# Optimization experiments

Measured on AMD Instinct MI355X. Metric: run time of the kernel, lower is better.

## Reference

```python
import jax, jax.numpy as jnp
import numpy as np

PAD = 1
THRESH = 10.0


def setup_inputs() -> dict:
    key = jax.random.key(0)
    k1, k2, k3 = jax.random.split(key, 3)
    x = jax.random.normal(k1, (8, 16, 62, 62), dtype=jnp.float32)
    W = jax.random.normal(k2, (32, 16, 3, 3), dtype=jnp.float32)
    b = jax.random.normal(k3, (32,), dtype=jnp.float32)
    return {"x": x, "W": W, "b": b}


def reference(x, W, b):
    # ZeroPad2d(padding) on all four sides
    x = jnp.pad(x, ((0, 0), (0, 0), (PAD, PAD), (PAD, PAD)))
    T, C, xr, xc = x.shape
    O, _, wr, wc = W.shape
    L = xr * xc

    # get_xfft_thresh: 1D FFT over flattened HxW, zero coeffs with |Re| < thresh
    xf = jnp.fft.fft(x.reshape(T, C, L))                      # (T,C,L) complex
    xf = jnp.where(jnp.abs(xf.real) < THRESH, jnp.zeros_like(xf), xf)

    # get_Wfft: zero-pad kernel to (xr,xc) bottom/right, flatten, reverse along
    # length (flipud(flip([0,1])) nets to a flip of the last axis only), then FFT
    Wp = jnp.pad(W, ((0, 0), (0, 0), (0, xr - wr), (0, xc - wc))).reshape(O, C, L)
    Wf = jnp.fft.fft(Wp[:, :, ::-1])                          # (O,C,L) complex

    # fftConv1D, batched over (image, out_channel):
    y = jnp.fft.ifft(xf[:, None, :, :] * Wf[None, :, :, :]).real  # (T,O,C,L)
    # torch.roll(y, 1) with no dims rolls the FLATTENED (C*L) tensor by 1
    y = jnp.roll(y.reshape(T, O, C * L), 1, axis=-1).reshape(T, O, C, xr, xc)
    y = y.sum(axis=2)                                         # sum over in-channels
    ans_r, ans_c = xr - wr + 1, xc - wc + 1
    y = y[:, :, :ans_r, :ans_c]
    return y + b[None, :, None, None]
```

## Files before the change

### kernel.cpp

```cpp
#include <hip/hip_runtime.h>
#include <math.h>

#define TWO_PI 6.28318530717958647692f
#define NT     512
#define RPW    8
#define PITCH  65
#define THRESH 10.0f
#define C64    0.995184726672196886f
#define S64    0.098017140329560602f
#define C4096  0.999998823451701879f
#define S4096  0.001533980186284766f

typedef float v2f __attribute__((ext_vector_type(2)));

__device__ __forceinline__ int brev6(int x) {
    return (int)(__brev((unsigned)x) >> 26);
}

__device__ __forceinline__ v2f cmul_add(v2f a, v2f b, v2f acc) {
    acc += (v2f){a.x, a.x} * b;
    acc += (v2f){a.y, a.y} * (v2f){-b.y, b.x};
    return acc;
}

template<int R>
__device__ __forceinline__ void fft64_dif(float (&re)[R], float (&im)[R],
                                          int lane, float sign) {
    #pragma unroll
    for (int h = 32; h >= 1; h >>= 1) {
        int j = lane & (h - 1);
        float ang = sign * (TWO_PI / 64.0f) * (float)(j * (32 / h));
        float wr, wi;
        __sincosf(ang, &wi, &wr);
        bool upper = (lane & h) != 0;
        float cwr = upper ? wr : 1.0f;
        float cwi = upper ? wi : 0.0f;
        float sgn = upper ? -1.0f : 1.0f;
        #pragma unroll
        for (int m = 0; m < R; ++m) {
            float orr = __shfl_xor(re[m], h, 64);
            float oii = __shfl_xor(im[m], h, 64);
            float ar = fmaf(sgn, re[m], orr);
            float ai = fmaf(sgn, im[m], oii);
            re[m] = ar * cwr - ai * cwi;
            im[m] = ar * cwi + ai * cwr;
        }
    }
}

template<int R>
__device__ __forceinline__ void fft64_dit(float (&re)[R], float (&im)[R],
                                          int lane, float sign) {
    #pragma unroll
    for (int h = 1; h <= 32; h <<= 1) {
        int j = lane & (h - 1);
        float ang = sign * (TWO_PI / 64.0f) * (float)(j * (32 / h));
        float wr, wi;
        __sincosf(ang, &wi, &wr);
        bool upper = (lane & h) != 0;
        float cwr = upper ? wr : 1.0f;
        float cwi = upper ? wi : 0.0f;
        float sgn = upper ? -1.0f : 1.0f;
        #pragma unroll
        for (int m = 0; m < R; ++m) {
            float tr = re[m] * cwr - im[m] * cwi;
            float ti = re[m] * cwi + im[m] * cwr;
            float orr = __shfl_xor(tr, h, 64);
            float oii = __shfl_xor(ti, h, 64);
            re[m] = fmaf(sgn, tr, orr);
            im[m] = fmaf(sgn, ti, oii);
        }
    }
}

__global__ __launch_bounds__(NT) void fwdA_kernel(const float* __restrict__ x,
                                                  float2* __restrict__ Xa) {
    __shared__ float sre[64 * 33];
    __shared__ float sim[64 * 33];
    const int task = blockIdx.x >> 1;
    const int h    = blockIdx.x & 1;
    const int tid  = threadIdx.x;
    const int lane = tid & 63;
    const int w    = tid >> 6;
    const float* xr = x + (size_t)task * 62 * 62;
    for (int idx = tid; idx < 64 * 32; idx += NT) {
        int r = idx >> 5, j = idx & 31;
        int n2 = 32 * h + j;
        float v = 0.0f;
        if (r >= 1 && r <= 62 && n2 >= 1 && n2 <= 62)
            v = xr[(r - 1) * 62 + (n2 - 1)];
        sre[r * 33 + j] = v;
    }
    __syncthreads();
    float re[4], im[4];
    #pragma unroll
    for (int m = 0; m < 4; ++m) {
        re[m] = sre[lane * 33 + (w * 4 + m)];
        im[m] = 0.0f;
    }
    fft64_dif<4>(re, im, lane, -1.0f);
    __syncthreads();
    const int k1 = brev6(lane);
    #pragma unroll
    for (int m = 0; m < 4; ++m) {
        int j  = w * 4 + m;
        int n2 = 32 * h + j;
        float cr, ci;
        __sincosf(-(TWO_PI / 4096.0f) * (float)(k1 * n2), &ci, &cr);
        sre[k1 * 33 + j] = re[m] * cr - im[m] * ci;
        sim[k1 * 33 + j] = re[m] * ci + im[m] * cr;
    }
    __syncthreads();
    float2* Arow = Xa + (size_t)task * 4096;
    for (int idx = tid; idx < 64 * 32; idx += NT) {
        int k = idx >> 5, j = idx & 31;
        Arow[k * 64 + 32 * h + j] = make_float2(sre[k * 33 + j], sim[k * 33 + j]);
    }
}

__global__ __launch_bounds__(NT) void fwdB_kernel(const float2* __restrict__ Xa,
                                                  float2* __restrict__ X) {
    const int task = blockIdx.x >> 1;
    const int h    = blockIdx.x & 1;
    const int tid  = threadIdx.x;
    const int lane = tid & 63;
    const int w    = tid >> 6;
    const float2* Arow = Xa + (size_t)task * 4096;
    float re[4], im[4];
    #pragma unroll
    for (int m = 0; m < 4; ++m) {
        float2 xv = Arow[(32 * h + w * 4 + m) * 64 + lane];
        re[m] = xv.x; im[m] = xv.y;
    }
    fft64_dif<4>(re, im, lane, -1.0f);
    float2* Xrow = X + (size_t)task * 4096;
    #pragma unroll
    for (int m = 0; m < 4; ++m) {
        float rr = re[m], ii = im[m];
        if (fabsf(rr) < THRESH) { rr = 0.0f; ii = 0.0f; }
        Xrow[(32 * h + w * 4 + m) * 64 + lane] = make_float2(rr, ii);
    }
}

__global__ __launch_bounds__(NT, 2) void conv_kernel(const float2* __restrict__ X,
                                                     const float* __restrict__ W,
                                                     const float* __restrict__ b,
                                                     float* __restrict__ out) {
    __shared__ float sre[64 * PITCH];
    __shared__ float sim[64 * PITCH];
    const int t    = blockIdx.x >> 5;
    const int o    = blockIdx.x & 31;
    const int tid  = threadIdx.x;
    const int lane = tid & 63;
    const int w    = tid >> 6;

    const int k2 = brev6(lane);
    float elr, eli;
    __sincosf((TWO_PI / 64.0f) * (float)k2, &eli, &elr);

    v2f uv[RPW], vv[RPW], v2v[RPW];
    {
        float cur, cui, cvr, cvi;
        __sincosf((TWO_PI / 8.0f) * (float)w, &cui, &cur);
        __sincosf((TWO_PI / 512.0f) * (float)w, &cvi, &cvr);
        #pragma unroll
        for (int m = 0; m < RPW; ++m) {
            uv[m] = (v2f){cur, cui};
            float vvr = cvr * elr - cvi * eli;
            float vvi = cvr * eli + cvi * elr;
            vv[m]  = (v2f){vvr, vvi};
            v2v[m] = (v2f){vvr * vvr - vvi * vvi, 2.0f * vvr * vvi};
            float nur = cur * C64 - cui * S64;
            cui = cur * S64 + cui * C64; cur = nur;
            float nvr = cvr * C4096 - cvi * S4096;
            cvi = cvr * S4096 + cvi * C4096; cvr = nvr;
        }
    }

    v2f S[RPW];
    #pragma unroll
    for (int m = 0; m < RPW; ++m) S[m] = (v2f){0.0f, 0.0f};

    const float2* Xt = X + (size_t)t * 16 * 4096 + (w * (RPW * 64) + lane);
    const float*  wo = W + o * 144;

    v2f xb[RPW];
    #pragma unroll
    for (int m = 0; m < RPW; ++m) {
        float2 q = Xt[m * 64];
        xb[m] = (v2f){q.x, q.y};
    }
    #pragma unroll 1
    for (int c = 0; c < 16; ++c) {
        v2f xn[RPW];
        if (c < 15) {
            const float2* xp = Xt + (c + 1) * 4096;
            #pragma unroll
            for (int m = 0; m < RPW; ++m) {
                float2 q = xp[m * 64];
                xn[m] = (v2f){q.x, q.y};
            }
        }
        const float wa0 = wo[c*9+0], wa1 = wo[c*9+1], wa2 = wo[c*9+2];
        const float wa3 = wo[c*9+3], wa4 = wo[c*9+4], wa5 = wo[c*9+5];
        const float wa6 = wo[c*9+6], wa7 = wo[c*9+7], wa8 = wo[c*9+8];
        #pragma unroll
        for (int m = 0; m < RPW; ++m) {
            v2f v = vv[m], v2 = v2v[m], u = uv[m];
            v2f h0 = (v2f){wa0, 0.0f}; h0 += v * wa1; h0 += v2 * wa2;
            v2f h1 = (v2f){wa3, 0.0f}; h1 += v * wa4; h1 += v2 * wa5;
            v2f h2 = (v2f){wa6, 0.0f}; h2 += v * wa7; h2 += v2 * wa8;
            v2f in = cmul_add(u, h2, h1);
            v2f P  = cmul_add(u, in, h0);
            S[m]   = cmul_add(xb[m], P, S[m]);
        }
        #pragma unroll
        for (int m = 0; m < RPW; ++m) xb[m] = xn[m];
    }

    float re[RPW], im[RPW];
    #pragma unroll
    for (int m = 0; m < RPW; ++m) { re[m] = S[m].x; im[m] = S[m].y; }
    fft64_dit<RPW>(re, im, lane, +1.0f);
    {
        float cr, ci, sr, si;
        __sincosf((TWO_PI / 512.0f) * (float)(lane * w), &ci, &cr);
        __sincosf((TWO_PI / 4096.0f) * (float)lane, &si, &sr);
        #pragma unroll
        for (int m = 0; m < RPW; ++m) {
            float rr = re[m] * cr - im[m] * ci;
            im[m]    = re[m] * ci + im[m] * cr;
            re[m]    = rr;
            float nr = cr * sr - ci * si;
            ci = cr * si + ci * sr; cr = nr;
        }
    }
    #pragma unroll
    for (int m = 0; m < RPW; ++m) {
        int k1 = w * RPW + m;
        sre[k1 * PITCH + lane] = re[m];
        sim[k1 * PITCH + lane] = im[m];
    }
    __syncthreads();
    #pragma unroll
    for (int m = 0; m < RPW; ++m) {
        int n2 = w * RPW + m;
        re[m] = sre[lane * PITCH + n2];
        im[m] = sim[lane * PITCH + n2];
    }
    fft64_dif<RPW>(re, im, lane, +1.0f);
    __syncthreads();
    const int n1 = brev6(lane);
    #pragma unroll
    for (int m = 0; m < RPW; ++m) {
        int n2 = w * RPW + m;
        sre[n1 * PITCH + n2] = re[m];
    }
    __syncthreads();
    const float bias = b[o];
    float* orow = out + (size_t)blockIdx.x * 62 * 62;
    for (int idx = tid; idx < 62 * 62; idx += NT) {
        int r = idx / 62, s = idx - r * 62;
        orow[idx] = sre[r * PITCH + s] * (1.0f / 4096.0f) + bias;
    }
}

extern "C" void kernel_launch(void* const* d_in, const int* in_sizes, int n_in,
                              void* d_out, int out_size, void* d_ws, size_t ws_size,
                              hipStream_t stream) {
    const float* x = (const float*)d_in[0];
    const float* W = (const float*)d_in[1];
    const float* b = (const float*)d_in[2];
    float* out = (float*)d_out;
    float2* Xa = (float2*)d_ws;
    float2* X  = Xa + 128 * 4096;

    fwdA_kernel<<<dim3(256), dim3(NT), 0, stream>>>(x, Xa);
    fwdB_kernel<<<dim3(256), dim3(NT), 0, stream>>>(Xa, X);
    conv_kernel<<<dim3(256), dim3(NT), 0, stream>>>(X, W, b, out);
}
```

Before: 87.84 us.

## Fuse three FFT-conv stages into one cooperative kernel with grid syncs

Merges the two forward-FFT passes and the convolution/inverse-FFT pass into a single cooperative kernel launched with hipLaunchCooperativeKernel, separated by grid.sync() barriers. This removes two kernel launches and the gaps between them. In exchange it adds the cost of grid-wide barriers, and the shared memory is sized for the largest stage, which could limit occupancy. Correctness relies on all 256 blocks being co-resident.

```diff
diff --git a/kernel.cpp b/kernel.cpp
--- a/kernel.cpp
+++ b/kernel.cpp
@@ -1,5 +1,8 @@
 #include <hip/hip_runtime.h>
+#include <hip/hip_cooperative_groups.h>
 #include <math.h>
+
+namespace cg = cooperative_groups;
 
 #define TWO_PI 6.28318530717958647692f
 #define NT     512
@@ -73,195 +76,194 @@
     }
 }
 
-__global__ __launch_bounds__(NT) void fwdA_kernel(const float* __restrict__ x,
-                                                  float2* __restrict__ Xa) {
-    __shared__ float sre[64 * 33];
-    __shared__ float sim[64 * 33];
-    const int task = blockIdx.x >> 1;
-    const int h    = blockIdx.x & 1;
+__global__ __launch_bounds__(NT, 2) void fused_kernel(const float* __restrict__ x,
+                                                      const float* __restrict__ W,
+                                                      const float* __restrict__ b,
+                                                      float* __restrict__ out,
+                                                      float2* __restrict__ Xa,
+                                                      float2* __restrict__ X) {
+    cg::grid_group grid = cg::this_grid();
+    __shared__ float sre[64 * PITCH];
+    __shared__ float sim[64 * PITCH];
     const int tid  = threadIdx.x;
     const int lane = tid & 63;
     const int w    = tid >> 6;
-    const float* xr = x + (size_t)task * 62 * 62;
-    for (int idx = tid; idx < 64 * 32; idx += NT) {
-        int r = idx >> 5, j = idx & 31;
-        int n2 = 32 * h + j;
-        float v = 0.0f;
-        if (r >= 1 && r <= 62 && n2 >= 1 && n2 <= 62)
-            v = xr[(r - 1) * 62 + (n2 - 1)];
-        sre[r * 33 + j] = v;
-    }
-    __syncthreads();
-    float re[4], im[4];
-    #pragma unroll
-    for (int m = 0; m < 4; ++m) {
-        re[m] = sre[lane * 33 + (w * 4 + m)];
-        im[m] = 0.0f;
-    }
-    fft64_dif<4>(re, im, lane, -1.0f);
-    __syncthreads();
-    const int k1 = brev6(lane);
-    #pragma unroll
-    for (int m = 0; m < 4; ++m) {
-        int j  = w * 4 + m;
-        int n2 = 32 * h + j;
-        float cr, ci;
-        __sincosf(-(TWO_PI / 4096.0f) * (float)(k1 * n2), &ci, &cr);
-        sre[k1 * 33 + j] = re[m] * cr - im[m] * ci;
-        sim[k1 * 33 + j] = re[m] * ci + im[m] * cr;
-    }
-    __syncthreads();
-    float2* Arow = Xa + (size_t)task * 4096;
-    for (int idx = tid; idx < 64 * 32; idx += NT) {
-        int k = idx >> 5, j = idx & 31;
-        Arow[k * 64 + 32 * h + j] = make_float2(sre[k * 33 + j], sim[k * 33 + j]);
-    }
-}
-
-__global__ __launch_bounds__(NT) void fwdB_kernel(const float2* __restrict__ Xa,
-                                                  float2* __restrict__ X) {
-    const int task = blockIdx.x >> 1;
-    const int h    = blockIdx.x & 1;
-    const int tid  = threadIdx.x;
-    const int lane = tid & 63;
-    const int w    = tid >> 6;
-    const float2* Arow = Xa + (size_t)task * 4096;
-    float re[4], im[4];
-    #pragma unroll
-    for (int m = 0; m < 4; ++m) {
-        float2 xv = Arow[(32 * h + w * 4 + m) * 64 + lane];
-        re[m] = xv.x; im[m] = xv.y;
-    }
-    fft64_dif<4>(re, im, lane, -1.0f);
-    float2* Xrow = X + (size_t)task * 4096;
-    #pragma unroll
-    for (int m = 0; m < 4; ++m) {
-        float rr = re[m], ii = im[m];
-        if (fabsf(rr) < THRESH) { rr = 0.0f; ii = 0.0f; }
-        Xrow[(32 * h + w * 4 + m) * 64 + lane] = make_float2(rr, ii);
-    }
-}
-
-__global__ __launch_bounds__(NT, 2) void conv_kernel(const float2* __restrict__ X,
-                                                     const float* __restrict__ W,
-                                                     const float* __restrict__ b,
-                                                     float* __restrict__ out) {
-    __shared__ float sre[64 * PITCH];
-    __shared__ float sim[64 * PITCH];
-    const int t    = blockIdx.x >> 5;
-    const int o    = blockIdx.x & 31;
-    const int tid  = threadIdx.x;
-    const int lane = tid & 63;
-    const int w    = tid >> 6;
-
-    const int k2 = brev6(lane);
-    float elr, eli;
-    __sincosf((TWO_PI / 64.0f) * (float)k2, &eli, &elr);
-
-    v2f uv[RPW], vv[RPW], v2v[RPW];
+
     {
-        float cur, cui, cvr, cvi;
-        __sincosf((TWO_PI / 8.0f) * (float)w, &cui, &cur);
-        __sincosf((TWO_PI / 512.0f) * (float)w, &cvi, &cvr);
-        #pragma unroll
-        for (int m = 0; m < RPW; ++m) {
-            uv[m] = (v2f){cur, cui};
-            float vvr = cvr * elr - cvi * eli;
-            float vvi = cvr * eli + cvi * elr;
-            vv[m]  = (v2f){vvr, vvi};
-            v2v[m] = (v2f){vvr * vvr - vvi * vvi, 2.0f * vvr * vvi};
-            float nur = cur * C64 - cui * S64;
-            cui = cur * S64 + cui * C64; cur = nur;
-            float nvr = cvr * C4096 - cvi * S4096;
-            cvi = cvr * S4096 + cvi * C4096; cvr = nvr;
-        }
-    }
-
-    v2f S[RPW];
-    #pragma unroll
-    for (int m = 0; m < RPW; ++m) S[m] = (v2f){0.0f, 0.0f};
-
-    const float2* Xt = X + (size_t)t * 16 * 4096 + (w * (RPW * 64) + lane);
-    const float*  wo = W + o * 144;
-
-    v2f xb[RPW];
-    #pragma unroll
-    for (int m = 0; m < RPW; ++m) {
-        float2 q = Xt[m * 64];
-        xb[m] = (v2f){q.x, q.y};
-    }
-    #pragma unroll 1
-    for (int c = 0; c < 16; ++c) {
-        v2f xn[RPW];
-        if (c < 15) {
-            const float2* xp = Xt + (c + 1) * 4096;
+        const int task = blockIdx.x >> 1;
+        const int h    = blockIdx.x & 1;
+        const float* xr = x + (size_t)task * 62 * 62;
+        for (int idx = tid; idx < 64 * 32; idx += NT) {
+            int r = idx >> 5, j = idx & 31;
+            int n2 = 32 * h + j;
+            float v = 0.0f;
+            if (r >= 1 && r <= 62 && n2 >= 1 && n2 <= 62)
+                v = xr[(r - 1) * 62 + (n2 - 1)];
+            sre[r * 33 + j] = v;
+        }
+        __syncthreads();
+        float re[4], im[4];
+        #pragma unroll
+        for (int m = 0; m < 4; ++m) {
+            re[m] = sre[lane * 33 + (w * 4 + m)];
+            im[m] = 0.0f;
+        }
+        fft64_dif<4>(re, im, lane, -1.0f);
+        __syncthreads();
+        const int k1 = brev6(lane);
+        #pragma unroll
+        for (int m = 0; m < 4; ++m) {
+            int j  = w * 4 + m;
+            int n2 = 32 * h + j;
+            float cr, ci;
+            __sincosf(-(TWO_PI / 4096.0f) * (float)(k1 * n2), &ci, &cr);
+            sre[k1 * 33 + j] = re[m] * cr - im[m] * ci;
+            sim[k1 * 33 + j] = re[m] * ci + im[m] * cr;
+        }
+        __syncthreads();
+        float2* Arow = Xa + (size_t)task * 4096;
+        for (int idx = tid; idx < 64 * 32; idx += NT) {
+            int k = idx >> 5, j = idx & 31;
+            Arow[k * 64 + 32 * h + j] =
+                make_float2(sre[k * 33 + j], sim[k * 33 + j]);
+        }
+    }
+    grid.sync();
+
+    {
+        const int task = blockIdx.x >> 1;
+        const int h    = blockIdx.x & 1;
+        const float2* Arow = Xa + (size_t)task * 4096;
+        float re[4], im[4];
+        #pragma unroll
+        for (int m = 0; m < 4; ++m) {
+            float2 xv = Arow[(32 * h + w * 4 + m) * 64 + lane];
+            re[m] = xv.x; im[m] = xv.y;
+        }
+        fft64_dif<4>(re, im, lane, -1.0f);
+        float2* Xrow = X + (size_t)task * 4096;
+        #pragma unroll
+        for (int m = 0; m < 4; ++m) {
+            float rr = re[m], ii = im[m];
+            if (fabsf(rr) < THRESH) { rr = 0.0f; ii = 0.0f; }
+            Xrow[(32 * h + w * 4 + m) * 64 + lane] = make_float2(rr, ii);
+        }
+    }
+    grid.sync();
+
+    {
+        const int t    = blockIdx.x >> 5;
+        const int o    = blockIdx.x & 31;
+
+        const int k2 = brev6(lane);
+        float elr, eli;
+        __sincosf((TWO_PI / 64.0f) * (float)k2, &eli, &elr);
+
+        v2f uv[RPW], vv[RPW], v2v[RPW];
+        {
+            float cur, cui, cvr, cvi;
+            __sincosf((TWO_PI / 8.0f) * (float)w, &cui, &cur);
+            __sincosf((TWO_PI / 512.0f) * (float)w, &cvi, &cvr);
             #pragma unroll
             for (int m = 0; m < RPW; ++m) {
-                float2 q = xp[m * 64];
-                xn[m] = (v2f){q.x, q.y};
-            }
-        }
-        const float wa0 = wo[c*9+0], wa1 = wo[c*9+1], wa2 = wo[c*9+2];
-        const float wa3 = wo[c*9+3], wa4 = wo[c*9+4], wa5 = wo[c*9+5];
-        const float wa6 = wo[c*9+6], wa7 = wo[c*9+7], wa8 = wo[c*9+8];
-        #pragma unroll
-        for (int m = 0; m < RPW; ++m) {
-            v2f v = vv[m], v2 = v2v[m], u = uv[m];
-            v2f h0 = (v2f){wa0, 0.0f}; h0 += v * wa1; h0 += v2 * wa2;
-            v2f h1 = (v2f){wa3, 0.0f}; h1 += v * wa4; h1 += v2 * wa5;
-            v2f h2 = (v2f){wa6, 0.0f}; h2 += v * wa7; h2 += v2 * wa8;
-            v2f in = cmul_add(u, h2, h1);
-            v2f P  = cmul_add(u, in, h0);
-            S[m]   = cmul_add(xb[m], P, S[m]);
-        }
-        #pragma unroll
-        for (int m = 0; m < RPW; ++m) xb[m] = xn[m];
-    }
-
-    float re[RPW], im[RPW];
-    #pragma unroll
-    for (int m = 0; m < RPW; ++m) { re[m] = S[m].x; im[m] = S[m].y; }
-    fft64_dit<RPW>(re, im, lane, +1.0f);
-    {
-        float cr, ci, sr, si;
-        __sincosf((TWO_PI / 512.0f) * (float)(lane * w), &ci, &cr);
-        __sincosf((TWO_PI / 4096.0f) * (float)lane, &si, &sr);
-        #pragma unroll
-        for (int m = 0; m < RPW; ++m) {
-            float rr = re[m] * cr - im[m] * ci;
-            im[m]    = re[m] * ci + im[m] * cr;
-            re[m]    = rr;
-            float nr = cr * sr - ci * si;
-            ci = cr * si + ci * sr; cr = nr;
-        }
-    }
-    #pragma unroll
-    for (int m = 0; m < RPW; ++m) {
-        int k1 = w * RPW + m;
-        sre[k1 * PITCH + lane] = re[m];
-        sim[k1 * PITCH + lane] = im[m];
-    }
-    __syncthreads();
-    #pragma unroll
-    for (int m = 0; m < RPW; ++m) {
-        int n2 = w * RPW + m;
-        re[m] = sre[lane * PITCH + n2];
-        im[m] = sim[lane * PITCH + n2];
-    }
-    fft64_dif<RPW>(re, im, lane, +1.0f);
-    __syncthreads();
-    const int n1 = brev6(lane);
-    #pragma unroll
-    for (int m = 0; m < RPW; ++m) {
-        int n2 = w * RPW + m;
-        sre[n1 * PITCH + n2] = re[m];
-    }
-    __syncthreads();
-    const float bias = b[o];
-    float* orow = out + (size_t)blockIdx.x * 62 * 62;
-    for (int idx = tid; idx < 62 * 62; idx += NT) {
-        int r = idx / 62, s = idx - r * 62;
-        orow[idx] = sre[r * PITCH + s] * (1.0f / 4096.0f) + bias;
+                uv[m] = (v2f){cur, cui};
+                float vvr = cvr * elr - cvi * eli;
+                float vvi = cvr * eli + cvi * elr;
+                vv[m]  = (v2f){vvr, vvi};
+                v2v[m] = (v2f){vvr * vvr - vvi * vvi, 2.0f * vvr * vvi};
+                float nur = cur * C64 - cui * S64;
+                cui = cur * S64 + cui * C64; cur = nur;
+                float nvr = cvr * C4096 - cvi * S4096;
+                cvi = cvr * S4096 + cvi * C4096; cvr = nvr;
+            }
+        }
+
+        v2f S[RPW];
+        #pragma unroll
+        for (int m = 0; m < RPW; ++m) S[m] = (v2f){0.0f, 0.0f};
+
+        const float2* Xt = X + (size_t)t * 16 * 4096 + (w * (RPW * 64) + lane);
+        const float*  wo = W + o * 144;
+
+        v2f xb[RPW];
+        #pragma unroll
+        for (int m = 0; m < RPW; ++m) {
+            float2 q = Xt[m * 64];
+            xb[m] = (v2f){q.x, q.y};
+        }
+        #pragma unroll 1
+        for (int c = 0; c < 16; ++c) {
+            v2f xn[RPW];
+            if (c < 15) {
+                const float2* xp = Xt + (c + 1) * 4096;
+                #pragma unroll
+                for (int m = 0; m < RPW; ++m) {
+                    float2 q = xp[m * 64];
+                    xn[m] = (v2f){q.x, q.y};
+                }
+            }
+            const float wa0 = wo[c*9+0], wa1 = wo[c*9+1], wa2 = wo[c*9+2];
+            const float wa3 = wo[c*9+3], wa4 = wo[c*9+4], wa5 = wo[c*9+5];
+            const float wa6 = wo[c*9+6], wa7 = wo[c*9+7], wa8 = wo[c*9+8];
+            #pragma unroll
+            for (int m = 0; m < RPW; ++m) {
+                v2f v = vv[m], v2 = v2v[m], u = uv[m];
+                v2f h0 = (v2f){wa0, 0.0f}; h0 += v * wa1; h0 += v2 * wa2;
+                v2f h1 = (v2f){wa3, 0.0f}; h1 += v * wa4; h1 += v2 * wa5;
+                v2f h2 = (v2f){wa6, 0.0f}; h2 += v * wa7; h2 += v2 * wa8;
+                v2f in = cmul_add(u, h2, h1);
+                v2f P  = cmul_add(u, in, h0);
+                S[m]   = cmul_add(xb[m], P, S[m]);
+            }
+            #pragma unroll
+            for (int m = 0; m < RPW; ++m) xb[m] = xn[m];
+        }
+
+        float re[RPW], im[RPW];
+        #pragma unroll
+        for (int m = 0; m < RPW; ++m) { re[m] = S[m].x; im[m] = S[m].y; }
+        fft64_dit<RPW>(re, im, lane, +1.0f);
+        {
+            float cr, ci, sr, si;
+            __sincosf((TWO_PI / 512.0f) * (float)(lane * w), &ci, &cr);
+            __sincosf((TWO_PI / 4096.0f) * (float)lane, &si, &sr);
+            #pragma unroll
+            for (int m = 0; m < RPW; ++m) {
+                float rr = re[m] * cr - im[m] * ci;
+                im[m]    = re[m] * ci + im[m] * cr;
+                re[m]    = rr;
+                float nr = cr * sr - ci * si;
+                ci = cr * si + ci * sr; cr = nr;
+            }
+        }
+        #pragma unroll
+        for (int m = 0; m < RPW; ++m) {
+            int k1 = w * RPW + m;
+            sre[k1 * PITCH + lane] = re[m];
+            sim[k1 * PITCH + lane] = im[m];
+        }
+        __syncthreads();
+        #pragma unroll
+        for (int m = 0; m < RPW; ++m) {
+            int n2 = w * RPW + m;
+            re[m] = sre[lane * PITCH + n2];
+            im[m] = sim[lane * PITCH + n2];
+        }
+        fft64_dif<RPW>(re, im, lane, +1.0f);
+        __syncthreads();
+        const int n1 = brev6(lane);
+        #pragma unroll
+        for (int m = 0; m < RPW; ++m) {
+            int n2 = w * RPW + m;
+            sre[n1 * PITCH + n2] = re[m];
+        }
+        __syncthreads();
+        const float bias = b[o];
+        float* orow = out + (size_t)blockIdx.x * 62 * 62;
+        for (int idx = tid; idx < 62 * 62; idx += NT) {
+            int r = idx / 62, s = idx - r * 62;
+            orow[idx] = sre[r * PITCH + s] * (1.0f / 4096.0f) + bias;
+        }
     }
 }
 
@@ -275,7 +277,8 @@
     float2* Xa = (float2*)d_ws;
     float2* X  = Xa + 128 * 4096;
 
-    fwdA_kernel<<<dim3(256), dim3(NT), 0, stream>>>(x, Xa);
-    fwdB_kernel<<<dim3(256), dim3(NT), 0, stream>>>(Xa, X);
-    conv_kernel<<<dim3(256), dim3(NT), 0, stream>>>(X, W, b, out);
-}
+    void* args[] = { (void*)&x, (void*)&W, (void*)&b,
+                     (void*)&out, (void*)&Xa, (void*)&X };
+    hipLaunchCooperativeKernel((const void*)fused_kernel, dim3(256), dim3(NT),
+                               args, 0, stream);
+}
```

Result: slower. 157.9 us (+79.8%).
